# Optimization experiments

Hardware: AMD Instinct MI355X
Metric: run time of the kernel (lower is better)

## Reference

```python
import jax, jax.numpy as jnp
import numpy as np

B, S, H = 2, 2048, 2048
NH, NKV, HD = 16, 4, 128
THETA = 1000000.0

def _rope_tables(seq_len, dim, theta):
    inv_freq = 1.0 / (theta ** (np.arange(0, dim, 2, dtype=np.float32) / dim))
    t = np.arange(seq_len, dtype=np.float32)
    freqs = np.outer(t, inv_freq)                      # [S, dim/2]
    emb = np.concatenate([freqs, freqs], axis=-1)      # [S, dim]
    return jnp.asarray(np.cos(emb)), jnp.asarray(np.sin(emb))

def setup_inputs() -> dict:
    key = jax.random.key(0)
    ks = jax.random.split(key, 5)
    cos, sin = _rope_tables(S, HD, THETA)
    scale = 1.0 / np.sqrt(H)
    return {
        "x": jax.random.normal(ks[0], (B, S, H), jnp.float32),
        "cos": cos, "sin": sin,
        "wq": jax.random.normal(ks[1], (H, NH * HD), jnp.float32) * scale,
        "wk": jax.random.normal(ks[2], (H, NKV * HD), jnp.float32) * scale,
        "wv": jax.random.normal(ks[3], (H, NKV * HD), jnp.float32) * scale,
        "wo": jax.random.normal(ks[4], (NH * HD, H), jnp.float32) * scale,
    }

def _rotate_half(t):
    h = t.shape[-1] // 2
    return jnp.concatenate([-t[..., h:], t[..., :h]], axis=-1)

def reference(x, cos, sin, wq, wk, wv, wo):
    b, s, _ = x.shape
    n_rep = NH // NKV
    q = (x @ wq).reshape(b, s, NH, HD)    # [b,s,nh,hd]
    k = (x @ wk).reshape(b, s, NKV, HD)
    v = (x @ wv).reshape(b, s, NKV, HD)
    # RoPE: cos/sin [s,hd] broadcast over batch and heads
    c = cos[None, :, None, :]
    sn = sin[None, :, None, :]
    q = q * c + _rotate_half(q) * sn
    k = k * c + _rotate_half(k) * sn
    # GQA: repeat kv heads n_rep times
    k = jnp.repeat(k, n_rep, axis=2)      # [b,s,nh,hd]
    v = jnp.repeat(v, n_rep, axis=2)
    q = q.transpose(0, 2, 1, 3)           # [b,nh,s,hd]
    k = k.transpose(0, 2, 1, 3)
    v = v.transpose(0, 2, 1, 3)
    scores = jnp.einsum('bhqd,bhkd->bhqk', q, k) / jnp.sqrt(jnp.float32(HD))
    causal = jnp.tril(jnp.ones((s, s), dtype=bool))
    scores = jnp.where(causal[None, None], scores, jnp.float32(-jnp.inf))
    attn = jax.nn.softmax(scores.astype(jnp.float32), axis=-1).astype(q.dtype)
    out = jnp.einsum('bhqk,bhkd->bhqd', attn, v)
    out = out.transpose(0, 2, 1, 3).reshape(b, s, NH * HD)
    return out @ wo
```

## Files before the change

kernel.cpp:

```cpp
#include <hip/hip_runtime.h>
#include <hip/hip_bf16.h>

#define Bb 2
#define Ss 2048
#define Hh 2048
#define NH 16
#define NKV 4
#define HD 128
#define NREP (NH / NKV)
#define Mrows (Bb * Ss)
#define NQKV (NH*HD + 2*NKV*HD)

using short8 = __attribute__((ext_vector_type(8))) short;
using f32x4  = __attribute__((ext_vector_type(4))) float;

__device__ __forceinline__ unsigned short f2b(float f) {
  union { float f; unsigned u; } v; v.f = f;
  return (unsigned short)((v.u + 0x7fffu + ((v.u >> 16) & 1u)) >> 16);
}
__device__ __forceinline__ float b2f(unsigned short h) {
  union { unsigned u; float f; } v; v.u = ((unsigned)h) << 16; return v.f;
}

__device__ __forceinline__ void gload16(const void* g, void* l) {
  __builtin_amdgcn_global_load_lds(
      (const __attribute__((address_space(1))) unsigned int*)g,
      (__attribute__((address_space(3))) unsigned int*)l, 16, 0, 0);
}

__global__ void cvt_bf16(const float* __restrict__ in, unsigned short* __restrict__ out, int n) {
  int i = (blockIdx.x * blockDim.x + threadIdx.x) * 4;
  if (i < n) {
    float4 f = *(const float4*)(in + i);
    ushort4 o;
    o.x = f2b(f.x); o.y = f2b(f.y); o.z = f2b(f.z); o.w = f2b(f.w);
    *(ushort4*)(out + i) = o;
  }
}

__global__ void transpose_cvt(const float* __restrict__ in, unsigned short* __restrict__ out,
                              int R, int C) {
  __shared__ float tile[32][33];
  int c0 = blockIdx.x * 32, r0 = blockIdx.y * 32;
  int tx = threadIdx.x, ty = threadIdx.y;
  #pragma unroll
  for (int i = ty; i < 32; i += 8)
    tile[i][tx] = in[(long)(r0 + i) * C + c0 + tx];
  __syncthreads();
  #pragma unroll
  for (int i = ty; i < 32; i += 8)
    out[(long)(c0 + i) * R + r0 + tx] = f2b(tile[tx][i]);
}

template <bool OUT_BF16>
__global__ __launch_bounds__(256) void gemm_bt(const unsigned short* __restrict__ A,
                                               const unsigned short* __restrict__ Bt,
                                               void* __restrict__ Cv,
                                               int Mm, int Nn, int Kk) {
  __shared__ unsigned short As[128 * 32];
  __shared__ unsigned short Bs[128 * 32];
  const int t = threadIdx.x;
  const int lane = t & 63, wave = t >> 6;
  const int quad = lane >> 4, l16 = lane & 15;
  const int m0 = blockIdx.y * 128, n0 = blockIdx.x * 128;
  const int wm = (wave >> 1) * 64, wn = (wave & 1) * 64;

  f32x4 acc[4][4] = {};

  const unsigned short* Ag0 = A + (long)(m0 + (t >> 2)) * Kk + (t & 3) * 8;
  const unsigned short* Ag1 = A + (long)(m0 + 64 + (t >> 2)) * Kk + (t & 3) * 8;
  const unsigned short* Bg0 = Bt + (long)(n0 + (t >> 2)) * Kk + (t & 3) * 8;
  const unsigned short* Bg1 = Bt + (long)(n0 + 64 + (t >> 2)) * Kk + (t & 3) * 8;
  unsigned short* lA0 = As + (wave * 64) * 8;
  unsigned short* lA1 = As + (wave * 64 + 256) * 8;
  unsigned short* lB0 = Bs + (wave * 64) * 8;
  unsigned short* lB1 = Bs + (wave * 64 + 256) * 8;

  for (int k0 = 0; k0 < Kk; k0 += 32) {
    gload16(Ag0 + k0, lA0);
    gload16(Ag1 + k0, lA1);
    gload16(Bg0 + k0, lB0);
    gload16(Bg1 + k0, lB1);
    __syncthreads();

    short8 af[4], bf[4];
    #pragma unroll
    for (int i = 0; i < 4; i++)
      af[i] = *(const short8*)(As + (wm + i * 16 + l16) * 32 + quad * 8);
    #pragma unroll
    for (int i = 0; i < 4; i++)
      bf[i] = *(const short8*)(Bs + (wn + i * 16 + l16) * 32 + quad * 8);

    #pragma unroll
    for (int mi = 0; mi < 4; mi++)
      #pragma unroll
      for (int ni = 0; ni < 4; ni++)
        acc[mi][ni] = __builtin_amdgcn_mfma_f32_16x16x32_bf16(af[mi], bf[ni], acc[mi][ni], 0, 0, 0);
    __syncthreads();
  }

  #pragma unroll
  for (int mi = 0; mi < 4; mi++)
    #pragma unroll
    for (int ni = 0; ni < 4; ni++)
      #pragma unroll
      for (int r = 0; r < 4; r++) {
        long row = m0 + wm + mi * 16 + quad * 4 + r;
        long col = n0 + wn + ni * 16 + l16;
        if (OUT_BF16)
          ((unsigned short*)Cv)[row * Nn + col] = f2b(acc[mi][ni][r]);
        else
          ((float*)Cv)[row * Nn + col] = acc[mi][ni][r];
      }
}

__global__ void rope_qk(const unsigned short* __restrict__ qkv,
                        const float* __restrict__ cosT, const float* __restrict__ sinT,
                        unsigned short* __restrict__ qt, unsigned short* __restrict__ kt) {
  int row = blockIdx.x;
  int b = row >> 11, s = row & (Ss - 1);
  const unsigned short* r = qkv + (long)row * NQKV;
  for (int jj = threadIdx.x; jj < (NH + NKV) * 64; jj += 256) {
    int hh = jj >> 6, d = jj & 63;
    float c = cosT[s * HD + d], sn = sinT[s * HD + d];
    float x0 = b2f(r[hh * 128 + d]), x1 = b2f(r[hh * 128 + 64 + d]);
    float o0 = x0 * c - x1 * sn;
    float o1 = x1 * c + x0 * sn;
    if (hh < NH) {
      unsigned short* dst = qt + (((long)b * NH + hh) * Ss + s) * HD + d;
      dst[0] = f2b(o0); dst[64] = f2b(o1);
    } else {
      unsigned short* dst = kt + (((long)b * NKV + (hh - NH)) * Ss + s) * HD + d;
      dst[0] = f2b(o0); dst[64] = f2b(o1);
    }
  }
}

__global__ void vtrans(const unsigned short* __restrict__ qkv, unsigned short* __restrict__ vt) {
  __shared__ unsigned short tile[32][33];
  int bh = blockIdx.z;
  int b = bh >> 2, kvh = bh & 3;
  int d0 = blockIdx.y * 32, s0 = blockIdx.x * 32;
  int tx = threadIdx.x, ty = threadIdx.y;
  #pragma unroll
  for (int i = ty; i < 32; i += 8)
    tile[i][tx] = qkv[(long)(b * Ss + s0 + i) * NQKV + (NH + NKV) * HD + kvh * HD + d0 + tx];
  __syncthreads();
  #pragma unroll
  for (int i = ty; i < 32; i += 8)
    vt[((long)bh * HD + d0 + i) * Ss + s0 + tx] = tile[tx][i];
}

__global__ __launch_bounds__(256, 2) void flash_attn(const unsigned short* __restrict__ qt,
                                                     const unsigned short* __restrict__ kt,
                                                     const unsigned short* __restrict__ vt,
                                                     unsigned short* __restrict__ out) {
  __shared__ unsigned short Ks[2][64 * 128];
  __shared__ unsigned short Vs[2][128 * 64];

  const int w = threadIdx.x >> 6, lane = threadIdx.x & 63;
  const int quad = lane >> 4, l16 = lane & 15;
  const int r8 = lane >> 3, c8 = lane & 7;
  const int idx = blockIdx.x;
  const int t5 = idx >> 5;
  const int qblk = (idx < 256) ? (15 - t5) : (t5 - 8);
  const int bh = idx & 31;
  const int h = bh & (NH - 1), b = bh >> 4;
  const int q0w = qblk * 128 + w * 32;
  const int kvh = h / NREP;

  const unsigned short* Qb = qt + ((long)b * NH + h) * Ss * HD;
  const unsigned short* Kb = kt + ((long)b * NKV + kvh) * Ss * HD;
  const unsigned short* Vb = vt + ((long)b * NKV + kvh) * HD * Ss;
  const int nch = (qblk + 1) * 2;

  #pragma unroll
  for (int i = 0; i < 4; i++) {
    int rho = i * 16 + w * 4 + quad;
    int key = (rho & 32) + ((rho >> 2) & 3) * 8 + ((rho >> 4) & 1) * 4 + (rho & 3);
    int sg = l16 ^ (w * 4 + quad);
    gload16(Kb + (long)key * HD + sg * 8, &Ks[0][(i * 256 + w * 64) * 8]);
  }
  #pragma unroll
  for (int i = 0; i < 4; i++) {
    int dv = i * 32 + w * 8 + r8;
    int sg = c8 ^ r8;
    gload16(Vb + (long)dv * Ss + sg * 8, &Vs[0][(i * 256 + w * 64) * 8]);
  }

  short8 qf[2][4];
  #pragma unroll
  for (int qi = 0; qi < 2; qi++)
    #pragma unroll
    for (int kc = 0; kc < 4; kc++)
      qf[qi][kc] = *(const short8*)(Qb + (long)(q0w + qi * 16 + l16) * HD + kc * 32 + quad * 8);

  f32x4 accO[2][8] = {};
  float m_i[2], l_i[2];
  m_i[0] = m_i[1] = -__builtin_inff();
  l_i[0] = l_i[1] = 0.f;
  const float cscale = 1.4426950408889634f * 0.08838834764831845f;

  for (int c = 0; c < nch; ++c) {
    const unsigned short* Ksb = Ks[c & 1];
    const unsigned short* Vsb = Vs[c & 1];

    if (c + 1 < nch) {
      const int k0 = (c + 1) * 64;
      unsigned short* Kd = Ks[(c + 1) & 1];
      unsigned short* Vd = Vs[(c + 1) & 1];
      #pragma unroll
      for (int i = 0; i < 4; i++) {
        int rho = i * 16 + w * 4 + quad;
        int key = (rho & 32) + ((rho >> 2) & 3) * 8 + ((rho >> 4) & 1) * 4 + (rho & 3);
        int sg = l16 ^ (w * 4 + quad);
        gload16(Kb + (long)(k0 + key) * HD + sg * 8, Kd + (i * 256 + w * 64) * 8);
      }
      #pragma unroll
      for (int i = 0; i < 4; i++) {
        int dv = i * 32 + w * 8 + r8;
        int sg = c8 ^ r8;
        gload16(Vb + (long)dv * Ss + k0 + sg * 8, Vd + (i * 256 + w * 64) * 8);
      }
      asm volatile("s_waitcnt vmcnt(8)" ::: "memory");
    } else {
      asm volatile("s_waitcnt vmcnt(0)" ::: "memory");
    }
    asm volatile("s_barrier" ::: "memory");

    if (c * 64 < q0w + 32) {
      f32x4 sc[2][4] = {};
      #pragma unroll
      for (int T = 0; T < 4; T++)
        #pragma unroll
        for (int kc = 0; kc < 4; kc++) {
          short8 kf = *(const short8*)(Ksb + ((16 * T + l16) * 16 + ((kc * 4 + quad) ^ l16)) * 8);
          #pragma unroll
          for (int qi = 0; qi < 2; qi++)
            sc[qi][T] = __builtin_amdgcn_mfma_f32_16x16x32_bf16(kf, qf[qi][kc], sc[qi][T], 0, 0, 0);
        }

      if ((c + 1) * 64 - 1 > q0w) {
        #pragma unroll
        for (int qi = 0; qi < 2; qi++) {
          int qq = q0w + qi * 16 + l16;
          #pragma unroll
          for (int T = 0; T < 4; T++)
            #pragma unroll
            for (int r = 0; r < 4; r++) {
              int ka = c * 64 + (T >> 1) * 32 + quad * 8 + (T & 1) * 4 + r;
              if (ka > qq) sc[qi][T][r] = -__builtin_inff();
            }
        }
      }

      short8 pf[2][2];
      #pragma unroll
      for (int qi = 0; qi < 2; qi++) {
        float v = sc[qi][0][0];
        #pragma unroll
        for (int T = 0; T < 4; T++)
          #pragma unroll
          for (int r = 0; r < 4; r++) v = fmaxf(v, sc[qi][T][r]);
        v = fmaxf(v, __shfl_xor(v, 16));
        v = fmaxf(v, __shfl_xor(v, 32));
        float mn = fmaxf(m_i[qi], v);
        float alpha = __builtin_amdgcn_exp2f((m_i[qi] - mn) * cscale);
        m_i[qi] = mn;
        l_i[qi] *= alpha;
        #pragma unroll
        for (int Dt = 0; Dt < 8; Dt++)
          #pragma unroll
          for (int r = 0; r < 4; r++) accO[qi][Dt][r] *= alpha;

        float p[4][4], rs = 0.f;
        #pragma unroll
        for (int T = 0; T < 4; T++)
          #pragma unroll
          for (int r = 0; r < 4; r++) {
            p[T][r] = __builtin_amdgcn_exp2f((sc[qi][T][r] - mn) * cscale);
            rs += p[T][r];
          }
        rs += __shfl_xor(rs, 16);
        rs += __shfl_xor(rs, 32);
        l_i[qi] += rs;

        #pragma unroll
        for (int c2 = 0; c2 < 2; c2++) {
          short8 f;
          f[0] = (short)f2b(p[2 * c2][0]);     f[1] = (short)f2b(p[2 * c2][1]);
          f[2] = (short)f2b(p[2 * c2][2]);     f[3] = (short)f2b(p[2 * c2][3]);
          f[4] = (short)f2b(p[2 * c2 + 1][0]); f[5] = (short)f2b(p[2 * c2 + 1][1]);
          f[6] = (short)f2b(p[2 * c2 + 1][2]); f[7] = (short)f2b(p[2 * c2 + 1][3]);
          pf[qi][c2] = f;
        }
      }

      #pragma unroll
      for (int c2 = 0; c2 < 2; c2++)
        #pragma unroll
        for (int Dt = 0; Dt < 8; Dt++) {
          short8 vf = *(const short8*)(Vsb + ((16 * Dt + l16) * 8 + ((4 * c2 + quad) ^ (l16 & 7))) * 8);
          #pragma unroll
          for (int qi = 0; qi < 2; qi++)
            accO[qi][Dt] = __builtin_amdgcn_mfma_f32_16x16x32_bf16(vf, pf[qi][c2], accO[qi][Dt], 0, 0, 0);
        }
    }

    asm volatile("s_waitcnt lgkmcnt(0)" ::: "memory");
    asm volatile("s_barrier" ::: "memory");
  }

  #pragma unroll
  for (int qi = 0; qi < 2; qi++) {
    float inv = 1.f / l_i[qi];
    long orow = (long)b * Ss + q0w + qi * 16 + l16;
    #pragma unroll
    for (int Dt = 0; Dt < 8; Dt++) {
      ushort4 o;
      o.x = f2b(accO[qi][Dt][0] * inv);
      o.y = f2b(accO[qi][Dt][1] * inv);
      o.z = f2b(accO[qi][Dt][2] * inv);
      o.w = f2b(accO[qi][Dt][3] * inv);
      *(ushort4*)(out + orow * (NH * HD) + h * HD + Dt * 16 + quad * 4) = o;
    }
  }
}

extern "C" void kernel_launch(void* const* d_in, const int* in_sizes, int n_in,
                              void* d_out, int out_size, void* d_ws, size_t ws_size,
                              hipStream_t stream) {
  const float* x   = (const float*)d_in[0];
  const float* cosT = (const float*)d_in[1];
  const float* sinT = (const float*)d_in[2];
  const float* wq  = (const float*)d_in[3];
  const float* wk  = (const float*)d_in[4];
  const float* wv  = (const float*)d_in[5];
  const float* wo  = (const float*)d_in[6];
  float* out = (float*)d_out;

  char* ws = (char*)d_ws;
  unsigned short* xb    = (unsigned short*)(ws + 0);
  unsigned short* wqkvt = (unsigned short*)(ws + 16777216);
  unsigned short* wot   = (unsigned short*)(ws + 29360128);
  unsigned short* qkv   = (unsigned short*)(ws + 37748736);
  unsigned short* kt    = (unsigned short*)(ws + 62914560);
  unsigned short* vt    = (unsigned short*)(ws + 67108864);
  unsigned short* qtp   = xb;
  unsigned short* attno = qkv;

  cvt_bf16<<<Mrows * Hh / 4 / 256, 256, 0, stream>>>(x, xb, Mrows * Hh);

  dim3 tb(32, 8);
  transpose_cvt<<<dim3(Hh / 32, Hh / 32), tb, 0, stream>>>(wq, wqkvt, Hh, NH * HD);
  transpose_cvt<<<dim3(NKV * HD / 32, Hh / 32), tb, 0, stream>>>(wk, wqkvt + (long)NH * HD * Hh, Hh, NKV * HD);
  transpose_cvt<<<dim3(NKV * HD / 32, Hh / 32), tb, 0, stream>>>(wv, wqkvt + (long)(NH * HD + NKV * HD) * Hh, Hh, NKV * HD);
  transpose_cvt<<<dim3(Hh / 32, Hh / 32), tb, 0, stream>>>(wo, wot, Hh, Hh);

  gemm_bt<true><<<dim3(NQKV / 128, Mrows / 128), 256, 0, stream>>>(xb, wqkvt, qkv, Mrows, NQKV, Hh);

  rope_qk<<<Mrows, 256, 0, stream>>>(qkv, cosT, sinT, qtp, kt);
  vtrans<<<dim3(Ss / 32, HD / 32, Bb * NKV), tb, 0, stream>>>(qkv, vt);

  flash_attn<<<(Ss / 128) * NH * Bb, 256, 0, stream>>>(qtp, kt, vt, attno);

  gemm_bt<false><<<dim3(Hh / 128, Mrows / 128), 256, 0, stream>>>(attno, wot, out, Mrows, Hh, Hh);
}
```

Baseline: 343.4 us.

## Fuse RoPE and V transpose into QKV GEMM epilogue; pair causal q-blocks in attention

The QKV GEMM now uses a 128-row by full-head-width tile per block. Its epilogue applies RoPE and writes Q/K directly in head-major layout, and writes V transposed, which removes the separate rope and vtrans kernels and the intermediate QKV buffer round trip. Flash attention now has each block process two query tiles (j and 15-j) so every block does the same causal work, sharing K fragment loads across both; it runs at occupancy 1 with doubled accumulator registers. The three weight transposes are merged into one launch. Risks are register pressure and lower occupancy in attention, and strided scattered stores in the V epilogue.

Measured after the change: 383.4 us. +11.7%, slower.

```diff
diff --git a/kernel.cpp b/kernel.cpp
--- a/kernel.cpp
+++ b/kernel.cpp
@@ -18,9 +18,6 @@
   union { float f; unsigned u; } v; v.f = f;
   return (unsigned short)((v.u + 0x7fffu + ((v.u >> 16) & 1u)) >> 16);
 }
-__device__ __forceinline__ float b2f(unsigned short h) {
-  union { unsigned u; float f; } v; v.u = ((unsigned)h) << 16; return v.f;
-}
 
 __device__ __forceinline__ void gload16(const void* g, void* l) {
   __builtin_amdgcn_global_load_lds(
@@ -52,10 +49,125 @@
     out[(long)(c0 + i) * R + r0 + tx] = f2b(tile[tx][i]);
 }
 
-template <bool OUT_BF16>
+__global__ void transpose_qkv(const float* __restrict__ wq, const float* __restrict__ wk,
+                              const float* __restrict__ wv, unsigned short* __restrict__ outT) {
+  __shared__ float tile[32][33];
+  int n0 = blockIdx.x * 32, k0 = blockIdx.y * 32;
+  const float* src; int c0, C;
+  if (n0 < Hh)            { src = wq; c0 = n0;            C = NH * HD; }
+  else if (n0 < Hh + 512) { src = wk; c0 = n0 - Hh;       C = NKV * HD; }
+  else                    { src = wv; c0 = n0 - Hh - 512; C = NKV * HD; }
+  int tx = threadIdx.x, ty = threadIdx.y;
+  #pragma unroll
+  for (int i = ty; i < 32; i += 8)
+    tile[i][tx] = src[(long)(k0 + i) * C + c0 + tx];
+  __syncthreads();
+  #pragma unroll
+  for (int i = ty; i < 32; i += 8)
+    outT[(long)(n0 + i) * Hh + k0 + tx] = f2b(tile[tx][i]);
+}
+
+__global__ __launch_bounds__(256) void gemm_qkv(const unsigned short* __restrict__ A,
+                                                const unsigned short* __restrict__ Bt,
+                                                const float* __restrict__ cosT,
+                                                const float* __restrict__ sinT,
+                                                unsigned short* __restrict__ qt,
+                                                unsigned short* __restrict__ kt,
+                                                unsigned short* __restrict__ vt) {
+  __shared__ unsigned short As[128 * 32];
+  __shared__ unsigned short Bs[128 * 32];
+  const int t = threadIdx.x;
+  const int lane = t & 63, wave = t >> 6;
+  const int quad = lane >> 4, l16 = lane & 15;
+  const int tile = blockIdx.x;
+  const int n0 = tile * 128, m0 = blockIdx.y * 128;
+  const int wm = wave * 32;
+  const bool isv = tile >= 20;
+  const int Kk = Hh;
+
+  f32x4 acc[2][8] = {};
+
+  const unsigned short* Ag0 = A + (long)(m0 + (t >> 2)) * Kk + (t & 3) * 8;
+  const unsigned short* Ag1 = A + (long)(m0 + 64 + (t >> 2)) * Kk + (t & 3) * 8;
+  const unsigned short* Bg0 = Bt + (long)(n0 + (t >> 2)) * Kk + (t & 3) * 8;
+  const unsigned short* Bg1 = Bt + (long)(n0 + 64 + (t >> 2)) * Kk + (t & 3) * 8;
+  unsigned short* lA0 = As + (wave * 64) * 8;
+  unsigned short* lA1 = As + (wave * 64 + 256) * 8;
+  unsigned short* lB0 = Bs + (wave * 64) * 8;
+  unsigned short* lB1 = Bs + (wave * 64 + 256) * 8;
+
+  for (int k0 = 0; k0 < Kk; k0 += 32) {
+    gload16(Ag0 + k0, lA0);
+    gload16(Ag1 + k0, lA1);
+    gload16(Bg0 + k0, lB0);
+    gload16(Bg1 + k0, lB1);
+    __syncthreads();
+
+    short8 af[2], bf[8];
+    #pragma unroll
+    for (int i = 0; i < 2; i++)
+      af[i] = *(const short8*)(As + (wm + i * 16 + l16) * 32 + quad * 8);
+    #pragma unroll
+    for (int i = 0; i < 8; i++)
+      bf[i] = *(const short8*)(Bs + (i * 16 + l16) * 32 + quad * 8);
+
+    if (isv) {
+      #pragma unroll
+      for (int mi = 0; mi < 2; mi++)
+        #pragma unroll
+        for (int ni = 0; ni < 8; ni++)
+          acc[mi][ni] = __builtin_amdgcn_mfma_f32_16x16x32_bf16(bf[ni], af[mi], acc[mi][ni], 0, 0, 0);
+    } else {
+      #pragma unroll
+      for (int mi = 0; mi < 2; mi++)
+        #pragma unroll
+        for (int ni = 0; ni < 8; ni++)
+          acc[mi][ni] = __builtin_amdgcn_mfma_f32_16x16x32_bf16(af[mi], bf[ni], acc[mi][ni], 0, 0, 0);
+    }
+    __syncthreads();
+  }
+
+  if (!isv) {
+    const bool isq = tile < 16;
+    const int hh = isq ? tile : tile - 16;
+    #pragma unroll
+    for (int mi = 0; mi < 2; mi++)
+      #pragma unroll
+      for (int r = 0; r < 4; r++) {
+        int srow = m0 + wm + mi * 16 + quad * 4 + r;
+        int bb = srow >> 11, s = srow & (Ss - 1);
+        unsigned short* dst = isq ? qt + (((long)bb * NH + hh) * Ss + s) * HD
+                                  : kt + (((long)bb * NKV + hh) * Ss + s) * HD;
+        const float* cr = cosT + (long)s * HD;
+        const float* sr = sinT + (long)s * HD;
+        #pragma unroll
+        for (int ni = 0; ni < 4; ni++) {
+          int d = ni * 16 + l16;
+          float cc = cr[d], sn = sr[d];
+          float x0 = acc[mi][ni][r], x1 = acc[mi][ni + 4][r];
+          dst[d]      = f2b(x0 * cc - x1 * sn);
+          dst[d + 64] = f2b(x1 * cc + x0 * sn);
+        }
+      }
+  } else {
+    const int kvh = tile - 20;
+    const int bb = m0 >> 11;
+    #pragma unroll
+    for (int mi = 0; mi < 2; mi++)
+      #pragma unroll
+      for (int ni = 0; ni < 8; ni++)
+        #pragma unroll
+        for (int r = 0; r < 4; r++) {
+          int d = ni * 16 + quad * 4 + r;
+          int s = (m0 + wm + mi * 16 + l16) & (Ss - 1);
+          vt[(((long)bb * NKV + kvh) * HD + d) * Ss + s] = f2b(acc[mi][ni][r]);
+        }
+  }
+}
+
 __global__ __launch_bounds__(256) void gemm_bt(const unsigned short* __restrict__ A,
                                                const unsigned short* __restrict__ Bt,
-                                               void* __restrict__ Cv,
+                                               float* __restrict__ Cv,
                                                int Mm, int Nn, int Kk) {
   __shared__ unsigned short As[128 * 32];
   __shared__ unsigned short Bs[128 * 32];
@@ -107,51 +219,11 @@
       for (int r = 0; r < 4; r++) {
         long row = m0 + wm + mi * 16 + quad * 4 + r;
         long col = n0 + wn + ni * 16 + l16;
-        if (OUT_BF16)
-          ((unsigned short*)Cv)[row * Nn + col] = f2b(acc[mi][ni][r]);
-        else
-          ((float*)Cv)[row * Nn + col] = acc[mi][ni][r];
-      }
-}
-
-__global__ void rope_qk(const unsigned short* __restrict__ qkv,
-                        const float* __restrict__ cosT, const float* __restrict__ sinT,
-                        unsigned short* __restrict__ qt, unsigned short* __restrict__ kt) {
-  int row = blockIdx.x;
-  int b = row >> 11, s = row & (Ss - 1);
-  const unsigned short* r = qkv + (long)row * NQKV;
-  for (int jj = threadIdx.x; jj < (NH + NKV) * 64; jj += 256) {
-    int hh = jj >> 6, d = jj & 63;
-    float c = cosT[s * HD + d], sn = sinT[s * HD + d];
-    float x0 = b2f(r[hh * 128 + d]), x1 = b2f(r[hh * 128 + 64 + d]);
-    float o0 = x0 * c - x1 * sn;
-    float o1 = x1 * c + x0 * sn;
-    if (hh < NH) {
-      unsigned short* dst = qt + (((long)b * NH + hh) * Ss + s) * HD + d;
-      dst[0] = f2b(o0); dst[64] = f2b(o1);
-    } else {
-      unsigned short* dst = kt + (((long)b * NKV + (hh - NH)) * Ss + s) * HD + d;
-      dst[0] = f2b(o0); dst[64] = f2b(o1);
-    }
-  }
-}
-
-__global__ void vtrans(const unsigned short* __restrict__ qkv, unsigned short* __restrict__ vt) {
-  __shared__ unsigned short tile[32][33];
-  int bh = blockIdx.z;
-  int b = bh >> 2, kvh = bh & 3;
-  int d0 = blockIdx.y * 32, s0 = blockIdx.x * 32;
-  int tx = threadIdx.x, ty = threadIdx.y;
-  #pragma unroll
-  for (int i = ty; i < 32; i += 8)
-    tile[i][tx] = qkv[(long)(b * Ss + s0 + i) * NQKV + (NH + NKV) * HD + kvh * HD + d0 + tx];
-  __syncthreads();
-  #pragma unroll
-  for (int i = ty; i < 32; i += 8)
-    vt[((long)bh * HD + d0 + i) * Ss + s0 + tx] = tile[tx][i];
-}
-
-__global__ __launch_bounds__(256, 2) void flash_attn(const unsigned short* __restrict__ qt,
+        Cv[row * Nn + col] = acc[mi][ni][r];
+      }
+}
+
+__global__ __launch_bounds__(256, 1) void flash_attn(const unsigned short* __restrict__ qt,
                                                      const unsigned short* __restrict__ kt,
                                                      const unsigned short* __restrict__ vt,
                                                      unsigned short* __restrict__ out) {
@@ -161,18 +233,16 @@
   const int w = threadIdx.x >> 6, lane = threadIdx.x & 63;
   const int quad = lane >> 4, l16 = lane & 15;
   const int r8 = lane >> 3, c8 = lane & 7;
-  const int idx = blockIdx.x;
-  const int t5 = idx >> 5;
-  const int qblk = (idx < 256) ? (15 - t5) : (t5 - 8);
-  const int bh = idx & 31;
+  const int jj = blockIdx.x >> 5;
+  const int bh = blockIdx.x & 31;
   const int h = bh & (NH - 1), b = bh >> 4;
-  const int q0w = qblk * 128 + w * 32;
   const int kvh = h / NREP;
+  const int qs[2] = { jj * 128 + w * 32, (15 - jj) * 128 + w * 32 };
+  const int nch = 2 * (16 - jj);
 
   const unsigned short* Qb = qt + ((long)b * NH + h) * Ss * HD;
   const unsigned short* Kb = kt + ((long)b * NKV + kvh) * Ss * HD;
   const unsigned short* Vb = vt + ((long)b * NKV + kvh) * HD * Ss;
-  const int nch = (qblk + 1) * 2;
 
   #pragma unroll
   for (int i = 0; i < 4; i++) {
@@ -188,17 +258,22 @@
     gload16(Vb + (long)dv * Ss + sg * 8, &Vs[0][(i * 256 + w * 64) * 8]);
   }
 
-  short8 qf[2][4];
-  #pragma unroll
-  for (int qi = 0; qi < 2; qi++)
-    #pragma unroll
-    for (int kc = 0; kc < 4; kc++)
-      qf[qi][kc] = *(const short8*)(Qb + (long)(q0w + qi * 16 + l16) * HD + kc * 32 + quad * 8);
-
-  f32x4 accO[2][8] = {};
-  float m_i[2], l_i[2];
-  m_i[0] = m_i[1] = -__builtin_inff();
-  l_i[0] = l_i[1] = 0.f;
+  short8 qf[2][2][4];
+  #pragma unroll
+  for (int st = 0; st < 2; st++)
+    #pragma unroll
+    for (int qi = 0; qi < 2; qi++)
+      #pragma unroll
+      for (int kc = 0; kc < 4; kc++)
+        qf[st][qi][kc] = *(const short8*)(Qb + (long)(qs[st] + qi * 16 + l16) * HD + kc * 32 + quad * 8);
+
+  f32x4 accO[2][2][8] = {};
+  float m_i[2][2], l_i[2][2];
+  #pragma unroll
+  for (int st = 0; st < 2; st++) {
+    m_i[st][0] = m_i[st][1] = -__builtin_inff();
+    l_i[st][0] = l_i[st][1] = 0.f;
+  }
   const float cscale = 1.4426950408889634f * 0.08838834764831845f;
 
   for (int c = 0; c < nch; ++c) {
@@ -228,22 +303,33 @@
     }
     asm volatile("s_barrier" ::: "memory");
 
-    if (c * 64 < q0w + 32) {
+    const bool act0 = (c * 64 < qs[0] + 32);
+    const bool act1 = (c * 64 < qs[1] + 32);
+
+    short8 kf[4][4];
+    #pragma unroll
+    for (int T = 0; T < 4; T++)
+      #pragma unroll
+      for (int kc = 0; kc < 4; kc++)
+        kf[T][kc] = *(const short8*)(Ksb + ((16 * T + l16) * 16 + ((kc * 4 + quad) ^ l16)) * 8);
+
+    short8 pf[2][2][2];
+    #pragma unroll
+    for (int st = 0; st < 2; st++) {
+      if (!(st == 0 ? act0 : act1)) continue;
       f32x4 sc[2][4] = {};
       #pragma unroll
       for (int T = 0; T < 4; T++)
         #pragma unroll
-        for (int kc = 0; kc < 4; kc++) {
-          short8 kf = *(const short8*)(Ksb + ((16 * T + l16) * 16 + ((kc * 4 + quad) ^ l16)) * 8);
+        for (int kc = 0; kc < 4; kc++)
           #pragma unroll
           for (int qi = 0; qi < 2; qi++)
-            sc[qi][T] = __builtin_amdgcn_mfma_f32_16x16x32_bf16(kf, qf[qi][kc], sc[qi][T], 0, 0, 0);
-        }
-
-      if ((c + 1) * 64 - 1 > q0w) {
+            sc[qi][T] = __builtin_amdgcn_mfma_f32_16x16x32_bf16(kf[T][kc], qf[st][qi][kc], sc[qi][T], 0, 0, 0);
+
+      if ((c + 1) * 64 - 1 > qs[st]) {
         #pragma unroll
         for (int qi = 0; qi < 2; qi++) {
-          int qq = q0w + qi * 16 + l16;
+          int qq = qs[st] + qi * 16 + l16;
           #pragma unroll
           for (int T = 0; T < 4; T++)
             #pragma unroll
@@ -254,7 +340,6 @@
         }
       }
 
-      short8 pf[2][2];
       #pragma unroll
       for (int qi = 0; qi < 2; qi++) {
         float v = sc[qi][0][0];
@@ -264,105 +349,103 @@
           for (int r = 0; r < 4; r++) v = fmaxf(v, sc[qi][T][r]);
         v = fmaxf(v, __shfl_xor(v, 16));
         v = fmaxf(v, __shfl_xor(v, 32));
-        float mn = fmaxf(m_i[qi], v);
-        float alpha = __builtin_amdgcn_exp2f((m_i[qi] - mn) * cscale);
-        m_i[qi] = mn;
-        l_i[qi] *= alpha;
+        float mn = fmaxf(m_i[st][qi], v);
+        float alpha = __builtin_amdgcn_exp2f((m_i[st][qi] - mn) * cscale);
+        m_i[st][qi] = mn;
+        l_i[st][qi] *= alpha;
         #pragma unroll
         for (int Dt = 0; Dt < 8; Dt++)
           #pragma unroll
-          for (int r = 0; r < 4; r++) accO[qi][Dt][r] *= alpha;
-
-        float p[4][4], rs = 0.f;
+          for (int r = 0; r < 4; r++) accO[st][qi][Dt][r] *= alpha;
+
+        float rs = 0.f;
+        short8 f0, f1;
         #pragma unroll
         for (int T = 0; T < 4; T++)
           #pragma unroll
           for (int r = 0; r < 4; r++) {
-            p[T][r] = __builtin_amdgcn_exp2f((sc[qi][T][r] - mn) * cscale);
-            rs += p[T][r];
+            float p = __builtin_amdgcn_exp2f((sc[qi][T][r] - mn) * cscale);
+            rs += p;
+            if (T < 2) f0[(T & 1) * 4 + r] = (short)f2b(p);
+            else       f1[(T & 1) * 4 + r] = (short)f2b(p);
           }
         rs += __shfl_xor(rs, 16);
         rs += __shfl_xor(rs, 32);
-        l_i[qi] += rs;
-
-        #pragma unroll
-        for (int c2 = 0; c2 < 2; c2++) {
-          short8 f;
-          f[0] = (short)f2b(p[2 * c2][0]);     f[1] = (short)f2b(p[2 * c2][1]);
-          f[2] = (short)f2b(p[2 * c2][2]);     f[3] = (short)f2b(p[2 * c2][3]);
-          f[4] = (short)f2b(p[2 * c2 + 1][0]); f[5] = (short)f2b(p[2 * c2 + 1][1]);
-          f[6] = (short)f2b(p[2 * c2 + 1][2]); f[7] = (short)f2b(p[2 * c2 + 1][3]);
-          pf[qi][c2] = f;
+        l_i[st][qi] += rs;
+        pf[st][qi][0] = f0;
+        pf[st][qi][1] = f1;
+      }
+    }
+
+    #pragma unroll
+    for (int c2 = 0; c2 < 2; c2++)
+      #pragma unroll
+      for (int Dt = 0; Dt < 8; Dt++) {
+        short8 vf = *(const short8*)(Vsb + ((16 * Dt + l16) * 8 + ((4 * c2 + quad) ^ (l16 & 7))) * 8);
+        if (act0) {
+          #pragma unroll
+          for (int qi = 0; qi < 2; qi++)
+            accO[0][qi][Dt] = __builtin_amdgcn_mfma_f32_16x16x32_bf16(vf, pf[0][qi][c2], accO[0][qi][Dt], 0, 0, 0);
         }
-      }
-
-      #pragma unroll
-      for (int c2 = 0; c2 < 2; c2++)
-        #pragma unroll
-        for (int Dt = 0; Dt < 8; Dt++) {
-          short8 vf = *(const short8*)(Vsb + ((16 * Dt + l16) * 8 + ((4 * c2 + quad) ^ (l16 & 7))) * 8);
+        if (act1) {
           #pragma unroll
           for (int qi = 0; qi < 2; qi++)
-            accO[qi][Dt] = __builtin_amdgcn_mfma_f32_16x16x32_bf16(vf, pf[qi][c2], accO[qi][Dt], 0, 0, 0);
+            accO[1][qi][Dt] = __builtin_amdgcn_mfma_f32_16x16x32_bf16(vf, pf[1][qi][c2], accO[1][qi][Dt], 0, 0, 0);
         }
-    }
+      }
 
     asm volatile("s_waitcnt lgkmcnt(0)" ::: "memory");
     asm volatile("s_barrier" ::: "memory");
   }
 
   #pragma unroll
-  for (int qi = 0; qi < 2; qi++) {
-    float inv = 1.f / l_i[qi];
-    long orow = (long)b * Ss + q0w + qi * 16 + l16;
-    #pragma unroll
-    for (int Dt = 0; Dt < 8; Dt++) {
-      ushort4 o;
-      o.x = f2b(accO[qi][Dt][0] * inv);
-      o.y = f2b(accO[qi][Dt][1] * inv);
-      o.z = f2b(accO[qi][Dt][2] * inv);
-      o.w = f2b(accO[qi][Dt][3] * inv);
-      *(ushort4*)(out + orow * (NH * HD) + h * HD + Dt * 16 + quad * 4) = o;
+  for (int st = 0; st < 2; st++)
+    #pragma unroll
+    for (int qi = 0; qi < 2; qi++) {
+      float inv = 1.f / l_i[st][qi];
+      long orow = (long)b * Ss + qs[st] + qi * 16 + l16;
+      #pragma unroll
+      for (int Dt = 0; Dt < 8; Dt++) {
+        ushort4 o;
+        o.x = f2b(accO[st][qi][Dt][0] * inv);
+        o.y = f2b(accO[st][qi][Dt][1] * inv);
+        o.z = f2b(accO[st][qi][Dt][2] * inv);
+        o.w = f2b(accO[st][qi][Dt][3] * inv);
+        *(ushort4*)(out + orow * (NH * HD) + h * HD + Dt * 16 + quad * 4) = o;
+      }
     }
-  }
 }
 
 extern "C" void kernel_launch(void* const* d_in, const int* in_sizes, int n_in,
                               void* d_out, int out_size, void* d_ws, size_t ws_size,
                               hipStream_t stream) {
-  const float* x   = (const float*)d_in[0];
+  const float* x    = (const float*)d_in[0];
   const float* cosT = (const float*)d_in[1];
   const float* sinT = (const float*)d_in[2];
-  const float* wq  = (const float*)d_in[3];
-  const float* wk  = (const float*)d_in[4];
-  const float* wv  = (const float*)d_in[5];
-  const float* wo  = (const float*)d_in[6];
+  const float* wq   = (const float*)d_in[3];
+  const float* wk   = (const float*)d_in[4];
+  const float* wv   = (const float*)d_in[5];
+  const float* wo   = (const float*)d_in[6];
   float* out = (float*)d_out;
 
   char* ws = (char*)d_ws;
-  unsigned short* xb    = (unsigned short*)(ws + 0);
-  unsigned short* wqkvt = (unsigned short*)(ws + 16777216);
-  unsigned short* wot   = (unsigned short*)(ws + 29360128);
-  unsigned short* qkv   = (unsigned short*)(ws + 37748736);
-  unsigned short* kt    = (unsigned short*)(ws + 62914560);
-  unsigned short* vt    = (unsigned short*)(ws + 67108864);
-  unsigned short* qtp   = xb;
-  unsigned short* attno = qkv;
+  unsigned short* xb    = (unsigned short*)(ws);
+  unsigned short* wqkvt = (unsigned short*)(ws + (16l << 20));
+  unsigned short* wot   = (unsigned short*)(ws + (28l << 20));
+  unsigned short* qt    = (unsigned short*)(ws + (36l << 20));
+  unsigned short* kt    = (unsigned short*)(ws + (52l << 20));
+  unsigned short* vt    = (unsigned short*)(ws + (56l << 20));
+  unsigned short* attno = xb;
 
   cvt_bf16<<<Mrows * Hh / 4 / 256, 256, 0, stream>>>(x, xb, Mrows * Hh);
 
   dim3 tb(32, 8);
-  transpose_cvt<<<dim3(Hh / 32, Hh / 32), tb, 0, stream>>>(wq, wqkvt, Hh, NH * HD);
-  transpose_cvt<<<dim3(NKV * HD / 32, Hh / 32), tb, 0, stream>>>(wk, wqkvt + (long)NH * HD * Hh, Hh, NKV * HD);
-  transpose_cvt<<<dim3(NKV * HD / 32, Hh / 32), tb, 0, stream>>>(wv, wqkvt + (long)(NH * HD + NKV * HD) * Hh, Hh, NKV * HD);
+  transpose_qkv<<<dim3(NQKV / 32, Hh / 32), tb, 0, stream>>>(wq, wk, wv, wqkvt);
   transpose_cvt<<<dim3(Hh / 32, Hh / 32), tb, 0, stream>>>(wo, wot, Hh, Hh);
 
-  gemm_bt<true><<<dim3(NQKV / 128, Mrows / 128), 256, 0, stream>>>(xb, wqkvt, qkv, Mrows, NQKV, Hh);
-
-  rope_qk<<<Mrows, 256, 0, stream>>>(qkv, cosT, sinT, qtp, kt);
-  vtrans<<<dim3(Ss / 32, HD / 32, Bb * NKV), tb, 0, stream>>>(qkv, vt);
-
-  flash_attn<<<(Ss / 128) * NH * Bb, 256, 0, stream>>>(qtp, kt, vt, attno);
-
-  gemm_bt<false><<<dim3(Hh / 128, Mrows / 128), 256, 0, stream>>>(attno, wot, out, Mrows, Hh, Hh);
-}
+  gemm_qkv<<<dim3(NQKV / 128, Mrows / 128), 256, 0, stream>>>(xb, wqkvt, cosT, sinT, qt, kt, vt);
+
+  flash_attn<<<256, 256, 0, stream>>>(qt, kt, vt, attno);
+
+  gemm_bt<<<dim3(Hh / 128, Mrows / 128), 256, 0, stream>>>(attno, wot, out, Mrows, Hh, Hh);
+}
```
